# Kernel optimization log

Hardware: AMD Instinct MI355X
Metric: run time of the kernel (lower is better)

Reference implementation:

```python
import jax, jax.numpy as jnp
import numpy as np

C, V, T, B = 64, 16000, 64, 8
ALPHA = 1.0  # dt=None -> alpha = 1 (non-trainable buffer)


def setup_inputs() -> dict:
    key = jax.random.key(0)
    k0, k1, k2, k3 = jax.random.split(key, 4)
    tokens = jax.random.randint(k0, (T, B), 0, V)  # time-major [T, B]
    emb_ctx = jax.random.normal(k1, (V, C), dtype=jnp.float32)  # embedding2context
    emb_act = jax.random.normal(k2, (V, C), dtype=jnp.float32)  # embedding2actionable
    bound = 1.0 / np.sqrt(C)
    W_a = jax.random.uniform(k3, (C * V, C), dtype=jnp.float32, minval=-bound, maxval=bound)
    beta_mult = jnp.float32(1.0)
    beta_power = jnp.float32(1.0)
    return {"tokens": tokens, "emb_ctx": emb_ctx, "emb_act": emb_act,
            "W_a": W_a, "beta_mult": beta_mult, "beta_power": beta_power}


def reference(tokens, emb_ctx, emb_act, W_a, beta_mult, beta_power):
    Vv, Cc = emb_ctx.shape
    Tt, Bb = tokens.shape
    # W_a rows are indexed k = v*C + c after .view(-1, V, C)
    W3 = W_a.reshape(Vv, Cc, Cc)  # [V, C, C]

    def step(ctx, tok):
        ce = emb_ctx[tok]  # [B, C] context embedding
        ae = emb_act[tok]  # [B, C] actionable embedding
        ne = jnp.linalg.norm(ce, axis=1, keepdims=True)   # [B, 1]
        nc = jnp.linalg.norm(ctx, axis=1, keepdims=True)  # [B, 1]
        beta = ALPHA * (beta_mult * (ne / (ne + nc))) ** beta_power
        beta = jnp.clip(beta, 0.0, 1.0)
        ctx = (1.0 - beta) * ctx + beta * ce              # norm-gated blend
        # action_map[b,v,c] = sum_d W3[v,c,d] * ctx[b,d]; out[b,v] = sum_c am * ae
        am = jnp.einsum('vcd,bd->bvc', W3, ctx)           # [B, V, C]
        out = jnp.einsum('bvc,bc->bv', am, ae)            # [B, V]
        return ctx, out

    ctx0 = jnp.zeros((Bb, Cc), dtype=emb_ctx.dtype)
    _, outs = jax.lax.scan(step, ctx0, tokens)  # [T, B, V]
    return outs
```

## Files before the change

kernel.cpp:

```cpp
#include <hip/hip_runtime.h>
#include <hip/hip_bf16.h>
#include <stdint.h>

#define T_STEPS 64
#define B_SZ 8
#define C_DIM 64
#define V_SZ 16000
#define K_DIM 4096
#define M_ROWS 512
#define BN 64
#define BK 32
#define NITER (K_DIM / BK)
#define ATILE_BYTES 32768

typedef __bf16 bf16x8 __attribute__((ext_vector_type(8)));
typedef __bf16 bf16x4 __attribute__((ext_vector_type(4)));
typedef float f32x4 __attribute__((ext_vector_type(4)));

__global__ void ctx_kernel(const int* __restrict__ tokens,
                           const float* __restrict__ emb_ctx,
                           const float* __restrict__ beta_mult,
                           const float* __restrict__ beta_power,
                           float* __restrict__ ctx_hist) {
  const int b = blockIdx.x;
  const int d = threadIdx.x;
  const float bm = beta_mult[0];
  const float bp = beta_power[0];
  float ctx = 0.0f;
  for (int t = 0; t < T_STEPS; ++t) {
    const int tok = tokens[t * B_SZ + b];
    const float ce = emb_ctx[tok * C_DIM + d];
    float ne2 = ce * ce;
    float c2 = ctx * ctx;
#pragma unroll
    for (int s = 32; s > 0; s >>= 1) {
      ne2 += __shfl_xor(ne2, s, 64);
      c2 += __shfl_xor(c2, s, 64);
    }
    const float ne = sqrtf(ne2);
    const float nc = sqrtf(c2);
    float beta = powf(bm * (ne / (ne + nc)), bp);
    beta = fminf(fmaxf(beta, 0.0f), 1.0f);
    ctx = (1.0f - beta) * ctx + beta * ce;
    ctx_hist[(t * B_SZ + b) * C_DIM + d] = ctx;
  }
}

__global__ void build_m(const int* __restrict__ tokens,
                        const float* __restrict__ emb_act,
                        const float* __restrict__ ctx_hist,
                        char* __restrict__ Mblk) {
  const int m = blockIdx.x;
  const int tid = threadIdx.x;
  __shared__ float ctxs[C_DIM];
  __shared__ float aes[C_DIM];
  const int t = m >> 3, b = m & 7;
  const int tok = tokens[t * B_SZ + b];
  if (tid < C_DIM) {
    ctxs[tid] = ctx_hist[m * C_DIM + tid];
    aes[tid] = emb_act[tok * C_DIM + tid];
  }
  __syncthreads();
  const int c = tid >> 1;
  const int dh = (tid & 1) * 32;
  const float ae = aes[c];
#pragma unroll
  for (int q = 0; q < 4; ++q) {
    const int k0 = c * C_DIM + dh + q * 8;
    bf16x8 v;
#pragma unroll
    for (int jj = 0; jj < 8; ++jj) v[jj] = (__bf16)(ae * ctxs[dh + q * 8 + jj]);
    *(bf16x8*)(void*)(Mblk + (size_t)(k0 >> 5) * 32768 + ((k0 >> 3) & 3) * 8192 +
                      m * 16) = v;
  }
}

__global__ __launch_bounds__(512, 2)
void gemm_kernel(const char* __restrict__ Ablk, const float* __restrict__ W,
                 float* __restrict__ out) {
  __shared__ char wlds[4][4096];
  const int tid = threadIdx.x;
  const int lane = tid & 63;
  const int w = tid >> 6;
  const int lrow = lane & 15;
  const int g = lane >> 4;
  const int n0 = blockIdx.x * BN;

  int aoff[4];
#pragma unroll
  for (int fm = 0; fm < 4; ++fm)
    aoff[fm] = g * 8192 + (w * 64 + fm * 16 + lrow) * 16;

  const char* const Wc = (const char*)W;
  const size_t wvoff = ((size_t)(n0 + (tid >> 3)) * K_DIM + (tid & 7) * 4) * 4;
  const int wldsoff = ((tid & 7) >> 1) * 1024 + (tid >> 3) * 16 + (tid & 1) * 8;

  f32x4 acc[4][4];
#pragma unroll
  for (int fm = 0; fm < 4; ++fm)
#pragma unroll
    for (int fn = 0; fn < 4; ++fn) acc[fm][fn] = (f32x4){0.f, 0.f, 0.f, 0.f};

  bf16x8 a2[2][4];
  f32x4 wr[4];

  wr[0] = *(const f32x4*)(Wc + wvoff);
  wr[1] = *(const f32x4*)(Wc + wvoff + 128);
#pragma unroll
  for (int fm = 0; fm < 4; ++fm) a2[0][fm] = *(const bf16x8*)(Ablk + aoff[fm]);
  wr[2] = *(const f32x4*)(Wc + wvoff + 256);
  {
    bf16x4 h;
#pragma unroll
    for (int q = 0; q < 4; ++q) h[q] = (__bf16)wr[0][q];
    *(bf16x4*)(wlds[0] + wldsoff) = h;
  }
  asm volatile("s_waitcnt lgkmcnt(0)" ::: "memory");
  __builtin_amdgcn_s_barrier();
  __builtin_amdgcn_sched_barrier(0);

#pragma unroll 1
  for (int bb = 0; bb < NITER / 4; ++bb) {
#pragma unroll
    for (int j = 0; j < 4; ++j) {
      const int kt = bb * 4 + j;
      const int kta = (kt + 1 < NITER) ? kt + 1 : kt;
      const char* ap = Ablk + (size_t)kta * ATILE_BYTES;
#pragma unroll
      for (int fm = 0; fm < 4; ++fm)
        a2[(j + 1) & 1][fm] = *(const bf16x8*)(ap + aoff[fm]);
      const int ktw = (kt + 3 < NITER) ? kt + 3 : NITER - 1;
      wr[(j + 3) & 3] = *(const f32x4*)(Wc + wvoff + (size_t)ktw * 128);
      {
        bf16x4 h;
#pragma unroll
        for (int q = 0; q < 4; ++q) h[q] = (__bf16)wr[(j + 1) & 3][q];
        *(bf16x4*)(wlds[(j + 1) & 3] + wldsoff) = h;
      }
      asm volatile("s_waitcnt lgkmcnt(0)" ::: "memory");
      __builtin_amdgcn_s_barrier();
      __builtin_amdgcn_sched_barrier(0);
#pragma unroll
      for (int fn = 0; fn < 4; ++fn) {
        const bf16x8 bv =
            *(const bf16x8*)(wlds[j & 3] + g * 1024 + (fn * 16 + lrow) * 16);
#pragma unroll
        for (int fm = 0; fm < 4; ++fm)
          acc[fm][fn] = __builtin_amdgcn_mfma_f32_16x16x32_bf16(
              a2[j & 1][fm], bv, acc[fm][fn], 0, 0, 0);
      }
    }
  }

#pragma unroll
  for (int fm = 0; fm < 4; ++fm)
#pragma unroll
    for (int q = 0; q < 4; ++q) {
      const int row = w * 64 + fm * 16 + g * 4 + q;
      float* po = out + (size_t)row * V_SZ + n0 + lrow;
#pragma unroll
      for (int fn = 0; fn < 4; ++fn) po[fn * 16] = acc[fm][fn][q];
    }
}

extern "C" void kernel_launch(void* const* d_in, const int* in_sizes, int n_in,
                              void* d_out, int out_size, void* d_ws, size_t ws_size,
                              hipStream_t stream) {
  const int* tokens = (const int*)d_in[0];
  const float* emb_ctx = (const float*)d_in[1];
  const float* emb_act = (const float*)d_in[2];
  const float* W = (const float*)d_in[3];
  const float* beta_mult = (const float*)d_in[4];
  const float* beta_power = (const float*)d_in[5];
  float* out = (float*)d_out;

  char* Mblk = (char*)d_ws;
  float* ctx_hist = (float*)((char*)d_ws + (size_t)M_ROWS * K_DIM * 2);

  ctx_kernel<<<B_SZ, C_DIM, 0, stream>>>(tokens, emb_ctx, beta_mult, beta_power,
                                         ctx_hist);
  build_m<<<M_ROWS, 128, 0, stream>>>(tokens, emb_act, ctx_hist, Mblk);
  gemm_kernel<<<V_SZ / BN, 512, 0, stream>>>(Mblk, W, out);
}
```

Baseline: 175.0 us.

## Split GEMM M into two halves with XCD-aware block remap and nontemporal W loads

The GEMM grid doubles from 250 to 500 workgroups of 256 threads, each covering 256 of the 512 M rows. A blockIdx remap places both M-halves of the same N tile on the same XCD so the second read of that W tile can hit the shared L2. W loads are widened to 32 bytes per thread, marked nontemporal, and converted to bf16x8 LDS stores. The finer split fills the 256 CUs better, but each W column is now read and converted twice, and the L2 sharing depends on the remap matching the hardware's XCD dispatch order.

```diff
diff --git a/kernel.cpp b/kernel.cpp
--- a/kernel.cpp
+++ b/kernel.cpp
@@ -9,12 +9,13 @@
 #define K_DIM 4096
 #define M_ROWS 512
 #define BN 64
+#define BM 256
 #define BK 32
 #define NITER (K_DIM / BK)
 #define ATILE_BYTES 32768
+#define NWG 500
 
 typedef __bf16 bf16x8 __attribute__((ext_vector_type(8)));
-typedef __bf16 bf16x4 __attribute__((ext_vector_type(4)));
 typedef float f32x4 __attribute__((ext_vector_type(4)));
 
 __global__ void ctx_kernel(const int* __restrict__ tokens,
@@ -75,7 +76,7 @@
   }
 }
 
-__global__ __launch_bounds__(512, 2)
+__global__ __launch_bounds__(256, 2)
 void gemm_kernel(const char* __restrict__ Ablk, const float* __restrict__ W,
                  float* __restrict__ out) {
   __shared__ char wlds[4][4096];
@@ -84,16 +85,22 @@
   const int w = tid >> 6;
   const int lrow = lane & 15;
   const int g = lane >> 4;
-  const int n0 = blockIdx.x * BN;
+
+  const int orig = blockIdx.x;
+  const int xcd = orig & 7;
+  const int wg = ((xcd < 4) ? xcd * 63 : 4 * 63 + (xcd - 4) * 62) + (orig >> 3);
+  const int mi = wg & 1;
+  const int n0 = (wg >> 1) * BN;
+  const int m0 = mi * BM;
 
   int aoff[4];
 #pragma unroll
   for (int fm = 0; fm < 4; ++fm)
-    aoff[fm] = g * 8192 + (w * 64 + fm * 16 + lrow) * 16;
+    aoff[fm] = g * 8192 + (m0 + w * 64 + fm * 16 + lrow) * 16;
 
   const char* const Wc = (const char*)W;
-  const size_t wvoff = ((size_t)(n0 + (tid >> 3)) * K_DIM + (tid & 7) * 4) * 4;
-  const int wldsoff = ((tid & 7) >> 1) * 1024 + (tid >> 3) * 16 + (tid & 1) * 8;
+  const size_t wvoff = ((size_t)(n0 + (tid >> 2)) * K_DIM + (tid & 3) * 8) * 4;
+  const int wldsoff = (tid & 3) * 1024 + (tid >> 2) * 16;
 
   f32x4 acc[4][4];
 #pragma unroll
@@ -102,18 +109,21 @@
     for (int fn = 0; fn < 4; ++fn) acc[fm][fn] = (f32x4){0.f, 0.f, 0.f, 0.f};
 
   bf16x8 a2[2][4];
-  f32x4 wr[4];
-
-  wr[0] = *(const f32x4*)(Wc + wvoff);
-  wr[1] = *(const f32x4*)(Wc + wvoff + 128);
+  f32x4 wr[4][2];
+
+  wr[0][0] = __builtin_nontemporal_load((const f32x4*)(Wc + wvoff));
+  wr[0][1] = __builtin_nontemporal_load((const f32x4*)(Wc + wvoff + 16));
+  wr[1][0] = __builtin_nontemporal_load((const f32x4*)(Wc + wvoff + 128));
+  wr[1][1] = __builtin_nontemporal_load((const f32x4*)(Wc + wvoff + 144));
 #pragma unroll
   for (int fm = 0; fm < 4; ++fm) a2[0][fm] = *(const bf16x8*)(Ablk + aoff[fm]);
-  wr[2] = *(const f32x4*)(Wc + wvoff + 256);
+  wr[2][0] = __builtin_nontemporal_load((const f32x4*)(Wc + wvoff + 256));
+  wr[2][1] = __builtin_nontemporal_load((const f32x4*)(Wc + wvoff + 272));
   {
-    bf16x4 h;
-#pragma unroll
-    for (int q = 0; q < 4; ++q) h[q] = (__bf16)wr[0][q];
-    *(bf16x4*)(wlds[0] + wldsoff) = h;
+    bf16x8 h;
+#pragma unroll
+    for (int q = 0; q < 4; ++q) { h[q] = (__bf16)wr[0][0][q]; h[4 + q] = (__bf16)wr[0][1][q]; }
+    *(bf16x8*)(wlds[0] + wldsoff) = h;
   }
   asm volatile("s_waitcnt lgkmcnt(0)" ::: "memory");
   __builtin_amdgcn_s_barrier();
@@ -130,12 +140,18 @@
       for (int fm = 0; fm < 4; ++fm)
         a2[(j + 1) & 1][fm] = *(const bf16x8*)(ap + aoff[fm]);
       const int ktw = (kt + 3 < NITER) ? kt + 3 : NITER - 1;
-      wr[(j + 3) & 3] = *(const f32x4*)(Wc + wvoff + (size_t)ktw * 128);
+      wr[(j + 3) & 3][0] =
+          __builtin_nontemporal_load((const f32x4*)(Wc + wvoff + (size_t)ktw * 128));
+      wr[(j + 3) & 3][1] =
+          __builtin_nontemporal_load((const f32x4*)(Wc + wvoff + (size_t)ktw * 128 + 16));
       {
-        bf16x4 h;
-#pragma unroll
-        for (int q = 0; q < 4; ++q) h[q] = (__bf16)wr[(j + 1) & 3][q];
-        *(bf16x4*)(wlds[(j + 1) & 3] + wldsoff) = h;
+        bf16x8 h;
+#pragma unroll
+        for (int q = 0; q < 4; ++q) {
+          h[q] = (__bf16)wr[(j + 1) & 3][0][q];
+          h[4 + q] = (__bf16)wr[(j + 1) & 3][1][q];
+        }
+        *(bf16x8*)(wlds[(j + 1) & 3] + wldsoff) = h;
       }
       asm volatile("s_waitcnt lgkmcnt(0)" ::: "memory");
       __builtin_amdgcn_s_barrier();
@@ -156,7 +172,7 @@
   for (int fm = 0; fm < 4; ++fm)
 #pragma unroll
     for (int q = 0; q < 4; ++q) {
-      const int row = w * 64 + fm * 16 + g * 4 + q;
+      const int row = m0 + w * 64 + fm * 16 + g * 4 + q;
       float* po = out + (size_t)row * V_SZ + n0 + lrow;
 #pragma unroll
       for (int fn = 0; fn < 4; ++fn) po[fn * 16] = acc[fm][fn][q];
@@ -180,5 +196,5 @@
   ctx_kernel<<<B_SZ, C_DIM, 0, stream>>>(tokens, emb_ctx, beta_mult, beta_power,
                                          ctx_hist);
   build_m<<<M_ROWS, 128, 0, stream>>>(tokens, emb_act, ctx_hist, Mblk);
-  gemm_kernel<<<V_SZ / BN, 512, 0, stream>>>(Mblk, W, out);
-}
+  gemm_kernel<<<NWG, 256, 0, stream>>>(Mblk, W, out);
+}
```

New measurement: 208.9 us. 19.4% more time.

## Fuse outer-product A construction into GEMM and retile to 128x128 blocks

Applied to the files above, without the earlier changes.

Removes the separate kernel that materialized the ctx⊗ae bf16 operand and instead forms A tiles in registers from cached ctx rows and an LDS copy of the actionable embeddings. The GEMM is retiled to 128x128 blocks with 256 threads, each wave owning its own W LDS slice with a four-deep register ring and nontemporal loads. This drops a launch and the A round-trip through memory, but splits M into four tiles so W is streamed by multiple blocks and adds per-iteration conversion arithmetic.

```diff
diff --git a/kernel.cpp b/kernel.cpp
--- a/kernel.cpp
+++ b/kernel.cpp
@@ -8,13 +8,13 @@
 #define V_SZ 16000
 #define K_DIM 4096
 #define M_ROWS 512
-#define BN 64
+#define BM 128
+#define BN 128
 #define BK 32
 #define NITER (K_DIM / BK)
-#define ATILE_BYTES 32768
+#define NWG ((M_ROWS / BM) * (V_SZ / BN))
 
 typedef __bf16 bf16x8 __attribute__((ext_vector_type(8)));
-typedef __bf16 bf16x4 __attribute__((ext_vector_type(4)));
 typedef float f32x4 __attribute__((ext_vector_type(4)));
 
 __global__ void ctx_kernel(const int* __restrict__ tokens,
@@ -46,120 +46,138 @@
   }
 }
 
-__global__ void build_m(const int* __restrict__ tokens,
-                        const float* __restrict__ emb_act,
-                        const float* __restrict__ ctx_hist,
-                        char* __restrict__ Mblk) {
-  const int m = blockIdx.x;
-  const int tid = threadIdx.x;
-  __shared__ float ctxs[C_DIM];
-  __shared__ float aes[C_DIM];
-  const int t = m >> 3, b = m & 7;
-  const int tok = tokens[t * B_SZ + b];
-  if (tid < C_DIM) {
-    ctxs[tid] = ctx_hist[m * C_DIM + tid];
-    aes[tid] = emb_act[tok * C_DIM + tid];
-  }
-  __syncthreads();
-  const int c = tid >> 1;
-  const int dh = (tid & 1) * 32;
-  const float ae = aes[c];
-#pragma unroll
-  for (int q = 0; q < 4; ++q) {
-    const int k0 = c * C_DIM + dh + q * 8;
-    bf16x8 v;
-#pragma unroll
-    for (int jj = 0; jj < 8; ++jj) v[jj] = (__bf16)(ae * ctxs[dh + q * 8 + jj]);
-    *(bf16x8*)(void*)(Mblk + (size_t)(k0 >> 5) * 32768 + ((k0 >> 3) & 3) * 8192 +
-                      m * 16) = v;
-  }
-}
-
-__global__ __launch_bounds__(512, 2)
-void gemm_kernel(const char* __restrict__ Ablk, const float* __restrict__ W,
+__global__ __launch_bounds__(256, 2)
+void gemm_kernel(const int* __restrict__ tokens,
+                 const float* __restrict__ emb_act,
+                 const float* __restrict__ ctx_hist,
+                 const float* __restrict__ W,
                  float* __restrict__ out) {
-  __shared__ char wlds[4][4096];
+  __shared__ float ae_t[C_DIM][BM];
+  __shared__ char wlds[4][2][2048];
+
   const int tid = threadIdx.x;
   const int lane = tid & 63;
   const int w = tid >> 6;
   const int lrow = lane & 15;
   const int g = lane >> 4;
-  const int n0 = blockIdx.x * BN;
-
-  int aoff[4];
-#pragma unroll
-  for (int fm = 0; fm < 4; ++fm)
-    aoff[fm] = g * 8192 + (w * 64 + fm * 16 + lrow) * 16;
-
-  const char* const Wc = (const char*)W;
-  const size_t wvoff = ((size_t)(n0 + (tid >> 3)) * K_DIM + (tid & 7) * 4) * 4;
-  const int wldsoff = ((tid & 7) >> 1) * 1024 + (tid >> 3) * 16 + (tid & 1) * 8;
-
-  f32x4 acc[4][4];
-#pragma unroll
-  for (int fm = 0; fm < 4; ++fm)
-#pragma unroll
-    for (int fn = 0; fn < 4; ++fn) acc[fm][fn] = (f32x4){0.f, 0.f, 0.f, 0.f};
-
-  bf16x8 a2[2][4];
-  f32x4 wr[4];
-
-  wr[0] = *(const f32x4*)(Wc + wvoff);
-  wr[1] = *(const f32x4*)(Wc + wvoff + 128);
-#pragma unroll
-  for (int fm = 0; fm < 4; ++fm) a2[0][fm] = *(const bf16x8*)(Ablk + aoff[fm]);
-  wr[2] = *(const f32x4*)(Wc + wvoff + 256);
+
+  const int bid = blockIdx.x;
+  const int mi = bid & 3;
+  const int nj = bid >> 2;
+  const int m0 = mi * BM;
+  const int n0 = nj * BN + w * 32;
+
   {
-    bf16x4 h;
-#pragma unroll
-    for (int q = 0; q < 4; ++q) h[q] = (__bf16)wr[0][q];
-    *(bf16x4*)(wlds[0] + wldsoff) = h;
-  }
-  asm volatile("s_waitcnt lgkmcnt(0)" ::: "memory");
-  __builtin_amdgcn_s_barrier();
-  __builtin_amdgcn_sched_barrier(0);
+    const int m = tid & 127;
+    const int c0 = (tid >> 7) * 32;
+    const int tok = tokens[m0 + m];
+    const float* ap = emb_act + (size_t)tok * C_DIM + c0;
+#pragma unroll
+    for (int i = 0; i < 32; ++i) ae_t[c0 + i][m] = ap[i];
+  }
+
+  bf16x8 ctxr[8][2];
+#pragma unroll
+  for (int fm = 0; fm < 8; ++fm)
+#pragma unroll
+    for (int h = 0; h < 2; ++h) {
+      const float* cp =
+          ctx_hist + (size_t)(m0 + fm * 16 + lrow) * C_DIM + h * 32 + g * 8;
+      const f32x4 c0 = *(const f32x4*)cp;
+      const f32x4 c1 = *(const f32x4*)(cp + 4);
+      bf16x8 v;
+#pragma unroll
+      for (int j = 0; j < 4; ++j) {
+        v[j] = (__bf16)c0[j];
+        v[4 + j] = (__bf16)c1[j];
+      }
+      ctxr[fm][h] = v;
+    }
+
+  __syncthreads();
+
+  const float* const wp =
+      W + (size_t)(n0 + (lane >> 1)) * K_DIM + (lane & 1) * 16;
+  char* const wbase = &wlds[w][0][0] + (lane >> 1) * 16;
+  const int gw = (lane & 1) * 2;
+
+  f32x4 ring[4][4];
+#pragma unroll
+  for (int s = 0; s < 4; ++s) {
+    const float* p = wp + s * BK;
+#pragma unroll
+    for (int q = 0; q < 4; ++q)
+      ring[s][q] = __builtin_nontemporal_load((const f32x4*)(p + q * 4));
+  }
+
+  auto WSTORE = [&](int rs, int ls) {
+    bf16x8 w0, w1;
+#pragma unroll
+    for (int j = 0; j < 4; ++j) {
+      w0[j] = (__bf16)ring[rs][0][j];
+      w0[4 + j] = (__bf16)ring[rs][1][j];
+      w1[j] = (__bf16)ring[rs][2][j];
+      w1[4 + j] = (__bf16)ring[rs][3][j];
+    }
+    char* d = wbase + ls * 2048;
+    *(bf16x8*)(d + gw * 512) = w0;
+    *(bf16x8*)(d + (gw + 1) * 512) = w1;
+  };
+
+  WSTORE(0, 0);
+
+  f32x4 acc[8][2];
+#pragma unroll
+  for (int fm = 0; fm < 8; ++fm)
+#pragma unroll
+    for (int fn = 0; fn < 2; ++fn) acc[fm][fn] = (f32x4){0.f, 0.f, 0.f, 0.f};
+
+  float aev[8];
 
 #pragma unroll 1
-  for (int bb = 0; bb < NITER / 4; ++bb) {
-#pragma unroll
-    for (int j = 0; j < 4; ++j) {
-      const int kt = bb * 4 + j;
-      const int kta = (kt + 1 < NITER) ? kt + 1 : kt;
-      const char* ap = Ablk + (size_t)kta * ATILE_BYTES;
-#pragma unroll
-      for (int fm = 0; fm < 4; ++fm)
-        a2[(j + 1) & 1][fm] = *(const bf16x8*)(ap + aoff[fm]);
-      const int ktw = (kt + 3 < NITER) ? kt + 3 : NITER - 1;
-      wr[(j + 3) & 3] = *(const f32x4*)(Wc + wvoff + (size_t)ktw * 128);
+  for (int p = 0; p < NITER / 4; ++p) {
+#pragma unroll
+    for (int u = 0; u < 4; ++u) {
+      const int kt = p * 4 + u;
       {
-        bf16x4 h;
-#pragma unroll
-        for (int q = 0; q < 4; ++q) h[q] = (__bf16)wr[(j + 1) & 3][q];
-        *(bf16x4*)(wlds[(j + 1) & 3] + wldsoff) = h;
-      }
-      asm volatile("s_waitcnt lgkmcnt(0)" ::: "memory");
-      __builtin_amdgcn_s_barrier();
-      __builtin_amdgcn_sched_barrier(0);
-#pragma unroll
-      for (int fn = 0; fn < 4; ++fn) {
-        const bf16x8 bv =
-            *(const bf16x8*)(wlds[j & 3] + g * 1024 + (fn * 16 + lrow) * 16);
-#pragma unroll
-        for (int fm = 0; fm < 4; ++fm)
-          acc[fm][fn] = __builtin_amdgcn_mfma_f32_16x16x32_bf16(
-              a2[j & 1][fm], bv, acc[fm][fn], 0, 0, 0);
-      }
-    }
-  }
-
-#pragma unroll
-  for (int fm = 0; fm < 4; ++fm)
+        const int ktl = (kt + 4 < NITER) ? kt + 4 : NITER - 1;
+        const float* pp = wp + (size_t)ktl * BK;
+#pragma unroll
+        for (int q = 0; q < 4; ++q)
+          ring[u][q] = __builtin_nontemporal_load((const f32x4*)(pp + q * 4));
+      }
+      WSTORE((u + 1) & 3, (kt + 1) & 1);
+      if ((u & 1) == 0) {
+#pragma unroll
+        for (int fm = 0; fm < 8; ++fm) aev[fm] = ae_t[kt >> 1][fm * 16 + lrow];
+      }
+      const char* rb = &wlds[w][kt & 1][0];
+      const bf16x8 bv0 = *(const bf16x8*)(rb + g * 512 + lrow * 16);
+      const bf16x8 bv1 = *(const bf16x8*)(rb + g * 512 + (16 + lrow) * 16);
+      const int half = kt & 1;
+#pragma unroll
+      for (int fm = 0; fm < 8; ++fm) {
+        const float av = aev[fm];
+        const bf16x8 cx = ctxr[fm][half];
+        bf16x8 af;
+#pragma unroll
+        for (int j = 0; j < 8; ++j) af[j] = (__bf16)(av * (float)cx[j]);
+        acc[fm][0] =
+            __builtin_amdgcn_mfma_f32_16x16x32_bf16(af, bv0, acc[fm][0], 0, 0, 0);
+        acc[fm][1] =
+            __builtin_amdgcn_mfma_f32_16x16x32_bf16(af, bv1, acc[fm][1], 0, 0, 0);
+      }
+    }
+  }
+
+#pragma unroll
+  for (int fm = 0; fm < 8; ++fm)
 #pragma unroll
     for (int q = 0; q < 4; ++q) {
-      const int row = w * 64 + fm * 16 + g * 4 + q;
+      const int row = m0 + fm * 16 + g * 4 + q;
       float* po = out + (size_t)row * V_SZ + n0 + lrow;
 #pragma unroll
-      for (int fn = 0; fn < 4; ++fn) po[fn * 16] = acc[fm][fn][q];
+      for (int fn = 0; fn < 2; ++fn) po[fn * 16] = acc[fm][fn][q];
     }
 }
 
@@ -174,11 +192,9 @@
   const float* beta_power = (const float*)d_in[5];
   float* out = (float*)d_out;
 
-  char* Mblk = (char*)d_ws;
-  float* ctx_hist = (float*)((char*)d_ws + (size_t)M_ROWS * K_DIM * 2);
+  float* ctx_hist = (float*)d_ws;
 
   ctx_kernel<<<B_SZ, C_DIM, 0, stream>>>(tokens, emb_ctx, beta_mult, beta_power,
                                          ctx_hist);
-  build_m<<<M_ROWS, 128, 0, stream>>>(tokens, emb_act, ctx_hist, Mblk);
-  gemm_kernel<<<V_SZ / BN, 512, 0, stream>>>(Mblk, W, out);
+  gemm_kernel<<<NWG, 256, 0, stream>>>(tokens, emb_act, ctx_hist, W, out);
 }
```

Result: slower. 438.6 us (+150.6%).

## Retile GEMM to 128x128 blocks with direct global-to-LDS triple buffering

Applied to the files above, without the earlier changes.

Restructures the GEMM from full-M-by-64-column tiles into 128x128 tiles across 500 workgroups, remapped so that neighbouring tiles share XCDs. Both A and W tiles are staged into LDS with global_load_lds in a three-buffer pipeline, and W is converted from fp32 to bf16 after the LDS read using an XOR-swizzled layout. This removes the register round-trip and per-iteration conversion stores, but W is now read from HBM four times, once per M-block, and the fp32 W tile doubles LDS traffic.

```diff
diff --git a/kernel.cpp b/kernel.cpp
--- a/kernel.cpp
+++ b/kernel.cpp
@@ -8,14 +8,23 @@
 #define V_SZ 16000
 #define K_DIM 4096
 #define M_ROWS 512
-#define BN 64
+#define BM 128
+#define BN 128
 #define BK 32
 #define NITER (K_DIM / BK)
-#define ATILE_BYTES 32768
+#define NWG ((M_ROWS / BM) * (V_SZ / BN))
+#define ABYTES 8192
+#define WBYTES 16384
+#define BUFBYTES (ABYTES + WBYTES)
 
 typedef __bf16 bf16x8 __attribute__((ext_vector_type(8)));
-typedef __bf16 bf16x4 __attribute__((ext_vector_type(4)));
 typedef float f32x4 __attribute__((ext_vector_type(4)));
+
+__device__ __forceinline__ void gll16(const void* g, void* l) {
+  __builtin_amdgcn_global_load_lds(
+      (const __attribute__((address_space(1))) void*)g,
+      (__attribute__((address_space(3))) void*)l, 16, 0, 0);
+}
 
 __global__ void ctx_kernel(const int* __restrict__ tokens,
                            const float* __restrict__ emb_ctx,
@@ -75,89 +84,103 @@
   }
 }
 
-__global__ __launch_bounds__(512, 2)
+__global__ __launch_bounds__(256, 2)
 void gemm_kernel(const char* __restrict__ Ablk, const float* __restrict__ W,
                  float* __restrict__ out) {
-  __shared__ char wlds[4][4096];
+  __shared__ __align__(16) char smem[3][BUFBYTES];
   const int tid = threadIdx.x;
   const int lane = tid & 63;
   const int w = tid >> 6;
+  const int wm = w >> 1, wn = w & 1;
   const int lrow = lane & 15;
   const int g = lane >> 4;
-  const int n0 = blockIdx.x * BN;
-
-  int aoff[4];
+
+  const int orig = blockIdx.x;
+  const int xcd = orig & 7;
+  const int wg = ((xcd < 4) ? xcd * 63 : 252 + (xcd - 4) * 62) + (orig >> 3);
+  const int m0 = (wg & 3) * BM;
+  const int n0 = (wg >> 2) * BN;
+
+  const char* const abase =
+      Ablk + (tid >> 7) * 8192 + (size_t)(m0 + (tid & 127)) * 16;
+  const char* const Wc = (const char*)W;
+  const int woff = ((tid & 7) * 16) ^ (((tid >> 3) & 7) << 4);
+  const char* wbase[4];
+#pragma unroll
+  for (int s = 0; s < 4; ++s)
+    wbase[s] = Wc + (size_t)(n0 + s * 32 + (tid >> 3)) * (K_DIM * 4) + woff;
+
+  auto STAGE = [&](int b, int kt) {
+    char* dst = smem[b];
+#pragma unroll
+    for (int s = 0; s < 2; ++s)
+      gll16(abase + (size_t)kt * 32768 + s * 16384, dst + s * 4096 + tid * 16);
+#pragma unroll
+    for (int s = 0; s < 4; ++s)
+      gll16(wbase[s] + (size_t)kt * 128, dst + ABYTES + s * 4096 + tid * 16);
+  };
+
+  f32x4 acc[4][4];
 #pragma unroll
   for (int fm = 0; fm < 4; ++fm)
-    aoff[fm] = g * 8192 + (w * 64 + fm * 16 + lrow) * 16;
-
-  const char* const Wc = (const char*)W;
-  const size_t wvoff = ((size_t)(n0 + (tid >> 3)) * K_DIM + (tid & 7) * 4) * 4;
-  const int wldsoff = ((tid & 7) >> 1) * 1024 + (tid >> 3) * 16 + (tid & 1) * 8;
-
-  f32x4 acc[4][4];
+#pragma unroll
+    for (int fn = 0; fn < 4; ++fn) acc[fm][fn] = (f32x4){0.f, 0.f, 0.f, 0.f};
+
+  auto COMPUTE = [&](int b) {
+    const char* Ab = smem[b];
+    const char* Wb = smem[b] + ABYTES;
+    bf16x8 a[4];
+#pragma unroll
+    for (int fm = 0; fm < 4; ++fm)
+      a[fm] = *(const bf16x8*)(Ab + g * 2048 + (wm * 64 + fm * 16 + lrow) * 16);
+#pragma unroll
+    for (int fn = 0; fn < 4; ++fn) {
+      const int col = wn * 64 + fn * 16 + lrow;
+      const int xo = (col & 7) << 4;
+      const f32x4 b0 = *(const f32x4*)(Wb + col * 128 + ((g * 32) ^ xo));
+      const f32x4 b1 = *(const f32x4*)(Wb + col * 128 + ((g * 32 + 16) ^ xo));
+      bf16x8 bv;
+#pragma unroll
+      for (int j = 0; j < 4; ++j) {
+        bv[j] = (__bf16)b0[j];
+        bv[4 + j] = (__bf16)b1[j];
+      }
+#pragma unroll
+      for (int fm = 0; fm < 4; ++fm)
+        acc[fm][fn] =
+            __builtin_amdgcn_mfma_f32_16x16x32_bf16(a[fm], bv, acc[fm][fn], 0, 0, 0);
+    }
+  };
+
+  STAGE(0, 0);
+  STAGE(1, 1);
+
+  int cur = 0;
+#pragma unroll 1
+  for (int kt = 0; kt < NITER - 2; ++kt) {
+    const int stg = (cur == 0) ? 2 : cur - 1;
+    STAGE(stg, kt + 2);
+    asm volatile("s_waitcnt vmcnt(12)" ::: "memory");
+    __builtin_amdgcn_s_barrier();
+    COMPUTE(cur);
+    __builtin_amdgcn_s_barrier();
+    cur = (cur == 2) ? 0 : cur + 1;
+  }
+  asm volatile("s_waitcnt vmcnt(6)" ::: "memory");
+  __builtin_amdgcn_s_barrier();
+  COMPUTE(cur);
+  __builtin_amdgcn_s_barrier();
+  cur = (cur == 2) ? 0 : cur + 1;
+  asm volatile("s_waitcnt vmcnt(0)" ::: "memory");
+  __builtin_amdgcn_s_barrier();
+  COMPUTE(cur);
+
 #pragma unroll
   for (int fm = 0; fm < 4; ++fm)
 #pragma unroll
-    for (int fn = 0; fn < 4; ++fn) acc[fm][fn] = (f32x4){0.f, 0.f, 0.f, 0.f};
-
-  bf16x8 a2[2][4];
-  f32x4 wr[4];
-
-  wr[0] = *(const f32x4*)(Wc + wvoff);
-  wr[1] = *(const f32x4*)(Wc + wvoff + 128);
-#pragma unroll
-  for (int fm = 0; fm < 4; ++fm) a2[0][fm] = *(const bf16x8*)(Ablk + aoff[fm]);
-  wr[2] = *(const f32x4*)(Wc + wvoff + 256);
-  {
-    bf16x4 h;
-#pragma unroll
-    for (int q = 0; q < 4; ++q) h[q] = (__bf16)wr[0][q];
-    *(bf16x4*)(wlds[0] + wldsoff) = h;
-  }
-  asm volatile("s_waitcnt lgkmcnt(0)" ::: "memory");
-  __builtin_amdgcn_s_barrier();
-  __builtin_amdgcn_sched_barrier(0);
-
-#pragma unroll 1
-  for (int bb = 0; bb < NITER / 4; ++bb) {
-#pragma unroll
-    for (int j = 0; j < 4; ++j) {
-      const int kt = bb * 4 + j;
-      const int kta = (kt + 1 < NITER) ? kt + 1 : kt;
-      const char* ap = Ablk + (size_t)kta * ATILE_BYTES;
-#pragma unroll
-      for (int fm = 0; fm < 4; ++fm)
-        a2[(j + 1) & 1][fm] = *(const bf16x8*)(ap + aoff[fm]);
-      const int ktw = (kt + 3 < NITER) ? kt + 3 : NITER - 1;
-      wr[(j + 3) & 3] = *(const f32x4*)(Wc + wvoff + (size_t)ktw * 128);
-      {
-        bf16x4 h;
-#pragma unroll
-        for (int q = 0; q < 4; ++q) h[q] = (__bf16)wr[(j + 1) & 3][q];
-        *(bf16x4*)(wlds[(j + 1) & 3] + wldsoff) = h;
-      }
-      asm volatile("s_waitcnt lgkmcnt(0)" ::: "memory");
-      __builtin_amdgcn_s_barrier();
-      __builtin_amdgcn_sched_barrier(0);
-#pragma unroll
-      for (int fn = 0; fn < 4; ++fn) {
-        const bf16x8 bv =
-            *(const bf16x8*)(wlds[j & 3] + g * 1024 + (fn * 16 + lrow) * 16);
-#pragma unroll
-        for (int fm = 0; fm < 4; ++fm)
-          acc[fm][fn] = __builtin_amdgcn_mfma_f32_16x16x32_bf16(
-              a2[j & 1][fm], bv, acc[fm][fn], 0, 0, 0);
-      }
-    }
-  }
-
-#pragma unroll
-  for (int fm = 0; fm < 4; ++fm)
-#pragma unroll
     for (int q = 0; q < 4; ++q) {
-      const int row = w * 64 + fm * 16 + g * 4 + q;
-      float* po = out + (size_t)row * V_SZ + n0 + lrow;
+      const int row = m0 + wm * 64 + fm * 16 + g * 4 + q;
+      float* po = out + (size_t)row * V_SZ + n0 + wn * 64 + lrow;
 #pragma unroll
       for (int fn = 0; fn < 4; ++fn) po[fn * 16] = acc[fm][fn][q];
     }
@@ -180,5 +203,5 @@
   ctx_kernel<<<B_SZ, C_DIM, 0, stream>>>(tokens, emb_ctx, beta_mult, beta_power,
                                          ctx_hist);
   build_m<<<M_ROWS, 128, 0, stream>>>(tokens, emb_act, ctx_hist, Mblk);
-  gemm_kernel<<<V_SZ / BN, 512, 0, stream>>>(Mblk, W, out);
-}
+  gemm_kernel<<<NWG, 256, 0, stream>>>(Mblk, W, out);
+}
```

New measurement: 193.6 us. 1.11x slower.
